# Optimization experiments

Hardware: AMD Instinct MI355X
Metric: run time of the kernel (lower is better)

The kernel has to match this reference:

```python
import jax, jax.numpy as jnp
import numpy as np

B, T, C = 4, 2048, 1024
NQ, D = 8, C // 8  # n_query heads, head dim = n_embd // 8


def setup_inputs() -> dict:
    key = jax.random.key(0)
    ks = jax.random.split(key, 6)
    s = 0.02
    return {
        "x": jax.random.normal(ks[0], (B, T, C), dtype=jnp.float32),
        "Wk": jax.random.normal(ks[1], (C, D), dtype=jnp.float32) * s,
        "Wv": jax.random.normal(ks[2], (C, D), dtype=jnp.float32) * s,
        "Wq": jax.random.normal(ks[3], (NQ, C, D), dtype=jnp.float32) * s,
        "Wp": jax.random.normal(ks[4], (NQ * D, C), dtype=jnp.float32) * s,
        "bp": jnp.zeros((C,), dtype=jnp.float32),
    }


def reference(x, Wk, Wv, Wq, Wp, bp):
    b, t, c = x.shape
    scale = c ** -0.5  # original scales by n_embd**-0.5, not head-dim
    k = x @ Wk                                   # [B,T,D] shared across heads (MQA)
    v = x @ Wv                                   # [B,T,D]
    q = jnp.einsum("btc,qcd->bqtd", x, Wq)       # [B,NQ,T,D]
    wei = jnp.einsum("bqtd,bsd->bqts", q, k) * scale
    causal = jnp.tril(jnp.ones((t, t), dtype=bool))
    wei = jnp.where(causal, wei, -jnp.inf)
    wei = jax.nn.softmax(wei, axis=-1)
    out = jnp.einsum("bqts,bsd->btqd", wei, v)   # [B,T,NQ,D]
    out = out.reshape(b, t, -1)                  # concat heads -> [B,T,NQ*D]
    return out @ Wp + bp
```

## Files before the change

kernel.cpp:

```cpp
#include <hip/hip_runtime.h>
#include <hip/hip_bf16.h>
#include <cstddef>
#include <cstdint>

#define B 4
#define T 2048
#define C 1024
#define NQ 8
#define D 128
#define M_ROWS (B * T)
#define NTOT (2 * D + NQ * D)

typedef __bf16 bf16x8 __attribute__((ext_vector_type(8)));
typedef float  f32x4  __attribute__((ext_vector_type(4)));
typedef uint32_t u32x4 __attribute__((ext_vector_type(4)));

__device__ __forceinline__ ushort f2bf(float f) {
    union { float f; uint32_t u; } v; v.f = f;
    const uint32_t r = (v.u + 0x7fffu + ((v.u >> 16) & 1u)) >> 16;
    return (ushort)r;
}

__device__ __forceinline__ uint32_t cvt_pk_bf16(float lo, float hi) {
    uint32_t r;
    asm("v_cvt_pk_bf16_f32 %0, %1, %2" : "=v"(r) : "v"(lo), "v"(hi));
    return r;
}

__device__ __forceinline__ void gld_lds16(const ushort* g, ushort* lds_uniform) {
    __builtin_amdgcn_global_load_lds(
        (const __attribute__((address_space(1))) void*)g,
        (__attribute__((address_space(3))) void*)lds_uniform, 16, 0, 0);
}

__global__ __launch_bounds__(256) void xcvt(const float* __restrict__ x,
                                            ushort* __restrict__ xb) {
    const size_t i = ((size_t)blockIdx.x * 256 + threadIdx.x) * 8;
    const float4 a = *(const float4*)(x + i);
    const float4 b = *(const float4*)(x + i + 4);
    uint4 o;
    o.x = f2bf(a.x) | ((uint32_t)f2bf(a.y) << 16);
    o.y = f2bf(a.z) | ((uint32_t)f2bf(a.w) << 16);
    o.z = f2bf(b.x) | ((uint32_t)f2bf(b.y) << 16);
    o.w = f2bf(b.z) | ((uint32_t)f2bf(b.w) << 16);
    *(uint4*)(xb + i) = o;
}

__device__ __forceinline__ void wtrans_body(const float* __restrict__ src,
                                            ushort* __restrict__ dst, int NC,
                                            int bx, int by) {
    __shared__ ushort Ts[64][72];
    const int tid = threadIdx.x;
    const int k0 = by * 64, c0 = bx * 64;
    {
        const int r = tid >> 2, cq = tid & 3;
#pragma unroll
        for (int i = 0; i < 4; ++i) {
            const int cc = cq * 16 + i * 4;
            const float4 v = *(const float4*)(src + (size_t)(k0 + r) * NC + c0 + cc);
            uint2 o;
            o.x = f2bf(v.x) | ((uint32_t)f2bf(v.y) << 16);
            o.y = f2bf(v.z) | ((uint32_t)f2bf(v.w) << 16);
            *(uint2*)(&Ts[r][cc]) = o;
        }
    }
    __syncthreads();
    {
        const int n = tid >> 2, kq = tid & 3;
        ushort vv[16];
#pragma unroll
        for (int j = 0; j < 16; ++j) vv[j] = Ts[kq * 16 + j][n];
        uint4 o0, o1;
        o0.x = vv[0] | ((uint32_t)vv[1] << 16);  o0.y = vv[2] | ((uint32_t)vv[3] << 16);
        o0.z = vv[4] | ((uint32_t)vv[5] << 16);  o0.w = vv[6] | ((uint32_t)vv[7] << 16);
        o1.x = vv[8] | ((uint32_t)vv[9] << 16);  o1.y = vv[10] | ((uint32_t)vv[11] << 16);
        o1.z = vv[12] | ((uint32_t)vv[13] << 16); o1.w = vv[14] | ((uint32_t)vv[15] << 16);
        ushort* d = dst + (size_t)(c0 + n) * C + k0 + kq * 16;
        *(uint4*)d = o0;
        *(uint4*)(d + 8) = o1;
    }
}

__global__ __launch_bounds__(256) void wtrans_qkv(const float* __restrict__ Wk,
                                                  const float* __restrict__ Wv,
                                                  const float* __restrict__ Wq,
                                                  ushort* __restrict__ WcatT) {
    const int z = blockIdx.z;
    const float* src;
    int rbase;
    if (z == 0)      { src = Wk; rbase = 0; }
    else if (z == 1) { src = Wv; rbase = D; }
    else             { src = Wq + (size_t)(z - 2) * C * D; rbase = 2 * D + (z - 2) * D; }
    wtrans_body(src, WcatT + (size_t)rbase * C, D, blockIdx.x, blockIdx.y);
}

__global__ __launch_bounds__(256) void wtrans_p(const float* __restrict__ Wp,
                                                ushort* __restrict__ WpT) {
    wtrans_body(Wp, WpT, C, blockIdx.x, blockIdx.y);
}

__global__ __launch_bounds__(256) void vtrans(const ushort* __restrict__ qkv,
                                              ushort* __restrict__ vbT) {
    __shared__ ushort Ts[64][136];
    const int tid = threadIdx.x;
    const int kb0 = blockIdx.x * 64;
    {
        const int r = tid >> 2, cq = tid & 3;
        const ushort* src = qkv + (size_t)(kb0 + r) * NTOT + D;
#pragma unroll
        for (int i = 0; i < 4; ++i) {
            const int cc = (cq * 4 + i) * 8;
            *(uint4*)(&Ts[r][cc]) = *(const uint4*)(src + cc);
        }
    }
    __syncthreads();
    {
        const int d = tid >> 1, half = tid & 1;
        ushort vv[32];
#pragma unroll
        for (int k = 0; k < 32; ++k) vv[k] = Ts[half * 32 + k][d];
        uint32_t dw[16];
#pragma unroll
        for (int i = 0; i < 16; ++i) {
            const int p0 = 2 * i, p1 = 2 * i + 1;
            const int k0 = (p0 & 3) | (((p0 >> 3) & 3) << 2) | (((p0 >> 2) & 1) << 4);
            const int k1 = (p1 & 3) | (((p1 >> 3) & 3) << 2) | (((p1 >> 2) & 1) << 4);
            dw[i] = vv[k0] | ((uint32_t)vv[k1] << 16);
        }
        uint32_t* dst = (uint32_t*)(vbT + (size_t)d * M_ROWS + kb0 + half * 32);
#pragma unroll
        for (int i = 0; i < 4; ++i)
            *(uint4*)(dst + i * 4) = *(uint4*)(&dw[i * 4]);
    }
}

template <bool BF16_OUT>
__global__ __launch_bounds__(256) void gemm_mfma(const ushort* __restrict__ A,
                                                 const ushort* __restrict__ Bt,
                                                 void* __restrict__ Cout,
                                                 const float* __restrict__ bias,
                                                 const int Nout) {
    __shared__ ushort As[128 * 32];
    __shared__ ushort Bs[128 * 32];
    const int tid  = threadIdx.x;
    const int lane = tid & 63;
    const int w    = tid >> 6;
    const int col  = lane & 15;
    const int quad = lane >> 4;
    const int row0 = blockIdx.y * 128;
    const int col0 = blockIdx.x * 128;
    const int wm = w & 1, wn = w >> 1;

    const int srow = lane >> 2;
    const int skk  = (lane & 3) * 8;

    f32x4 acc[4][4];
#pragma unroll
    for (int i = 0; i < 4; ++i)
#pragma unroll
        for (int j = 0; j < 4; ++j) acc[i][j] = (f32x4){0.f, 0.f, 0.f, 0.f};

    for (int k0 = 0; k0 < C; k0 += 32) {
        __syncthreads();
#pragma unroll
        for (int j = 0; j < 2; ++j) {
            const int ci = w * 2 + j;
            const int r  = ci * 16 + srow;
            gld_lds16(A  + (size_t)(row0 + r) * C + k0 + skk, &As[ci * 512]);
            gld_lds16(Bt + (size_t)(col0 + r) * C + k0 + skk, &Bs[ci * 512]);
        }
        __syncthreads();

        bf16x8 af[4], bfr[4];
#pragma unroll
        for (int i = 0; i < 4; ++i)
            af[i] = *(const bf16x8*)&As[(wm * 64 + i * 16 + col) * 32 + quad * 8];
#pragma unroll
        for (int j = 0; j < 4; ++j)
            bfr[j] = *(const bf16x8*)&Bs[(wn * 64 + j * 16 + col) * 32 + quad * 8];
#pragma unroll
        for (int i = 0; i < 4; ++i)
#pragma unroll
            for (int j = 0; j < 4; ++j)
                acc[i][j] = __builtin_amdgcn_mfma_f32_16x16x32_bf16(af[i], bfr[j], acc[i][j], 0, 0, 0);
    }

#pragma unroll
    for (int i = 0; i < 4; ++i) {
#pragma unroll
        for (int r = 0; r < 4; ++r) {
            const int grow = row0 + wm * 64 + i * 16 + quad * 4 + r;
#pragma unroll
            for (int j = 0; j < 4; ++j) {
                const int gcol = col0 + wn * 64 + j * 16 + col;
                const float v = acc[i][j][r];
                if (BF16_OUT) {
                    ((ushort*)Cout)[(size_t)grow * Nout + gcol] = f2bf(v);
                } else {
                    ((float*)Cout)[(size_t)grow * Nout + gcol] = v + bias[gcol];
                }
            }
        }
    }
}

__global__ __launch_bounds__(256, 2) void attn_mfma(const ushort* __restrict__ qkv,
                                                    const ushort* __restrict__ vbT,
                                                    ushort* __restrict__ attb) {
    __shared__ ushort Ks[2][4][64][32];
    __shared__ ushort Vt[2][4][128][16];

    const int tid  = threadIdx.x;
    const int lane = tid & 63;
    const int w    = tid >> 6;
    const int col  = lane & 15;
    const int quad = lane >> 4;
    const int h    = blockIdx.y;
    const int b    = blockIdx.z;
    const int qb_i = ((b >> 1) & 1) ? (gridDim.x - 1 - blockIdx.x) : blockIdx.x;
    const int q0   = qb_i * 128;

    bf16x8 qf[2][4];
#pragma unroll
    for (int qs = 0; qs < 2; ++qs) {
        const ushort* qrow = qkv + (size_t)(b * T + q0 + w * 32 + qs * 16 + col) * NTOT + 2 * D + h * D;
#pragma unroll
        for (int kb2 = 0; kb2 < 4; ++kb2)
            qf[qs][kb2] = *(const bf16x8*)(qrow + kb2 * 32 + quad * 8);
    }

    const ushort* kbase = qkv + (size_t)b * T * NTOT;
    const ushort* vbase = vbT + (size_t)b * T;

    f32x4 O[2][8];
#pragma unroll
    for (int qs = 0; qs < 2; ++qs)
#pragma unroll
        for (int i = 0; i < 8; ++i) O[qs][i] = (f32x4){0.f, 0.f, 0.f, 0.f};
    float l_acc[2] = {0.f, 0.f};

    const int ntiles  = 2 * qb_i + 2;
    const int sk_key  = lane >> 2;
    const int sk_d    = (lane & 3) * 8;
    const int sv_d    = lane >> 1;
    const int sv_half = (lane & 1) * 8;
    const int kg0     = quad >> 1;
    const int ko      = (quad & 1) * 8;
    const float SC = 0.045084220f;

    auto stage = [&](int it, int bufi) {
        const int s0 = it * 64;
#pragma unroll
        for (int kg = 0; kg < 4; ++kg)
            gld_lds16(kbase + (size_t)(s0 + kg * 16 + sk_key) * NTOT + w * 32 + sk_d,
                      &Ks[bufi][w][kg * 16][0]);
#pragma unroll
        for (int i2 = 0; i2 < 4; ++i2)
            gld_lds16(vbase + (size_t)(i2 * 32 + sv_d) * M_ROWS + s0 + w * 16 + sv_half,
                      &Vt[bufi][w][i2 * 32][0]);
    };

    int cur = 0;
    stage(0, 0);
    __syncthreads();

    for (int it = 0; it < ntiles; ++it) {
        if (it + 1 < ntiles) stage(it + 1, cur ^ 1);

        const bool active = (w >= 2) || (it < ntiles - 1);
        if (active) {
            const int s0 = it * 64;

            f32x4 S[2][4];
#pragma unroll
            for (int qs = 0; qs < 2; ++qs)
#pragma unroll
                for (int sub = 0; sub < 4; ++sub) S[qs][sub] = (f32x4){0.f, 0.f, 0.f, 0.f};
#pragma unroll
            for (int sub = 0; sub < 4; ++sub) {
#pragma unroll
                for (int kb2 = 0; kb2 < 4; ++kb2) {
                    bf16x8 kf = *(const bf16x8*)(&Ks[cur][kb2][sub * 16 + col][quad * 8]);
                    S[0][sub] = __builtin_amdgcn_mfma_f32_16x16x32_bf16(kf, qf[0][kb2], S[0][sub], 0, 0, 0);
                    S[1][sub] = __builtin_amdgcn_mfma_f32_16x16x32_bf16(kf, qf[1][kb2], S[1][sub], 0, 0, 0);
                }
            }

            const bool diag = (it >= ntiles - 2);
            bf16x8 paf[2][2];
#pragma unroll
            for (int qs = 0; qs < 2; ++qs) {
                float p[4][4];
                if (diag) {
                    const int q = q0 + w * 32 + qs * 16 + col;
#pragma unroll
                    for (int sub = 0; sub < 4; ++sub)
#pragma unroll
                        for (int r = 0; r < 4; ++r) {
                            const int key = s0 + sub * 16 + quad * 4 + r;
                            const float sc = (key > q) ? -1e30f : S[qs][sub][r] * SC;
                            p[sub][r] = __builtin_amdgcn_exp2f(sc);
                        }
                } else {
#pragma unroll
                    for (int sub = 0; sub < 4; ++sub)
#pragma unroll
                        for (int r = 0; r < 4; ++r)
                            p[sub][r] = __builtin_amdgcn_exp2f(S[qs][sub][r] * SC);
                }
                float ls = 0.f;
#pragma unroll
                for (int sub = 0; sub < 4; ++sub)
                    ls += (p[sub][0] + p[sub][1]) + (p[sub][2] + p[sub][3]);
                l_acc[qs] += ls;

                u32x4 w0, w1;
                w0.x = cvt_pk_bf16(p[0][0], p[0][1]);
                w0.y = cvt_pk_bf16(p[0][2], p[0][3]);
                w0.z = cvt_pk_bf16(p[1][0], p[1][1]);
                w0.w = cvt_pk_bf16(p[1][2], p[1][3]);
                w1.x = cvt_pk_bf16(p[2][0], p[2][1]);
                w1.y = cvt_pk_bf16(p[2][2], p[2][3]);
                w1.z = cvt_pk_bf16(p[3][0], p[3][1]);
                w1.w = cvt_pk_bf16(p[3][2], p[3][3]);
                paf[qs][0] = __builtin_bit_cast(bf16x8, w0);
                paf[qs][1] = __builtin_bit_cast(bf16x8, w1);
            }

#pragma unroll
            for (int nt = 0; nt < 8; ++nt) {
                bf16x8 vf0 = *(const bf16x8*)(&Vt[cur][kg0][nt * 16 + col][ko]);
                bf16x8 vf1 = *(const bf16x8*)(&Vt[cur][2 + kg0][nt * 16 + col][ko]);
#pragma unroll
                for (int qs = 0; qs < 2; ++qs) {
                    O[qs][nt] = __builtin_amdgcn_mfma_f32_16x16x32_bf16(paf[qs][0], vf0, O[qs][nt], 0, 0, 0);
                    O[qs][nt] = __builtin_amdgcn_mfma_f32_16x16x32_bf16(paf[qs][1], vf1, O[qs][nt], 0, 0, 0);
                }
            }
        }

        __syncthreads();
        cur ^= 1;
    }

#pragma unroll
    for (int qs = 0; qs < 2; ++qs) {
        float s = l_acc[qs];
        s += __shfl_xor(s, 16);
        s += __shfl_xor(s, 32);
#pragma unroll
        for (int r = 0; r < 4; ++r) {
            const float inv = 1.0f / __shfl(s, quad * 4 + r);
            const int t = q0 + w * 32 + qs * 16 + quad * 4 + r;
            ushort* orow = attb + (size_t)(b * T + t) * C + h * D;
#pragma unroll
            for (int nt = 0; nt < 8; ++nt)
                orow[nt * 16 + col] = f2bf(O[qs][nt][r] * inv);
        }
    }
}

extern "C" void kernel_launch(void* const* d_in, const int* in_sizes, int n_in,
                              void* d_out, int out_size, void* d_ws, size_t ws_size,
                              hipStream_t stream) {
    const float* x  = (const float*)d_in[0];
    const float* Wk = (const float*)d_in[1];
    const float* Wv = (const float*)d_in[2];
    const float* Wq = (const float*)d_in[3];
    const float* Wp = (const float*)d_in[4];
    const float* bp = (const float*)d_in[5];
    float* out = (float*)d_out;

    char* ws = (char*)d_ws;
    ushort* xb    = (ushort*)ws;
    ushort* attb  = xb;
    ushort* qkv   = (ushort*)(ws + (size_t)16  * 1024 * 1024);
    ushort* WcatT = (ushort*)(ws + (size_t)36  * 1024 * 1024);
    ushort* WpT   = (ushort*)(ws + (size_t)39  * 1024 * 1024);
    ushort* vbT   = (ushort*)(ws + (size_t)41  * 1024 * 1024);

    xcvt<<<(size_t)M_ROWS * C / (256 * 8), 256, 0, stream>>>(x, xb);
    wtrans_qkv<<<dim3(D / 64, C / 64, 2 + NQ), 256, 0, stream>>>(Wk, Wv, Wq, WcatT);
    wtrans_p<<<dim3(C / 64, C / 64), 256, 0, stream>>>(Wp, WpT);

    gemm_mfma<true><<<dim3(NTOT / 128, M_ROWS / 128), 256, 0, stream>>>(
        xb, WcatT, qkv, nullptr, NTOT);

    vtrans<<<M_ROWS / 64, 256, 0, stream>>>(qkv, vbT);

    attn_mfma<<<dim3(T / 128, NQ, B), 256, 0, stream>>>(qkv, vbT, attb);

    gemm_mfma<false><<<dim3(C / 128, M_ROWS / 128), 256, 0, stream>>>(
        attb, WpT, out, bp, C);
}
```

Before: 211.6 us.

## Use two waves per attention block with 64 query rows each

```diff
diff --git a/kernel.cpp b/kernel.cpp
--- a/kernel.cpp
+++ b/kernel.cpp
@@ -204,7 +204,7 @@
     }
 }
 
-__global__ __launch_bounds__(256, 2) void attn_mfma(const ushort* __restrict__ qkv,
+__global__ __launch_bounds__(128, 2) void attn_mfma(const ushort* __restrict__ qkv,
                                                     const ushort* __restrict__ vbT,
                                                     ushort* __restrict__ attb) {
     __shared__ ushort Ks[2][4][64][32];
@@ -217,13 +217,13 @@
     const int quad = lane >> 4;
     const int h    = blockIdx.y;
     const int b    = blockIdx.z;
-    const int qb_i = ((b >> 1) & 1) ? (gridDim.x - 1 - blockIdx.x) : blockIdx.x;
+    const int qb_i = ((b >> 1) & 1) ? (15 - (int)blockIdx.x) : (int)blockIdx.x;
     const int q0   = qb_i * 128;
 
-    bf16x8 qf[2][4];
-#pragma unroll
-    for (int qs = 0; qs < 2; ++qs) {
-        const ushort* qrow = qkv + (size_t)(b * T + q0 + w * 32 + qs * 16 + col) * NTOT + 2 * D + h * D;
+    bf16x8 qf[4][4];
+#pragma unroll
+    for (int qs = 0; qs < 4; ++qs) {
+        const ushort* qrow = qkv + (size_t)(b * T + q0 + w * 64 + qs * 16 + col) * NTOT + 2 * D + h * D;
 #pragma unroll
         for (int kb2 = 0; kb2 < 4; ++kb2)
             qf[qs][kb2] = *(const bf16x8*)(qrow + kb2 * 32 + quad * 8);
@@ -232,12 +232,12 @@
     const ushort* kbase = qkv + (size_t)b * T * NTOT;
     const ushort* vbase = vbT + (size_t)b * T;
 
-    f32x4 O[2][8];
-#pragma unroll
-    for (int qs = 0; qs < 2; ++qs)
+    f32x4 O[4][8];
+#pragma unroll
+    for (int qs = 0; qs < 4; ++qs)
 #pragma unroll
         for (int i = 0; i < 8; ++i) O[qs][i] = (f32x4){0.f, 0.f, 0.f, 0.f};
-    float l_acc[2] = {0.f, 0.f};
+    float l_acc[4] = {0.f, 0.f, 0.f, 0.f};
 
     const int ntiles  = 2 * qb_i + 2;
     const int sk_key  = lane >> 2;
@@ -251,13 +251,17 @@
     auto stage = [&](int it, int bufi) {
         const int s0 = it * 64;
 #pragma unroll
-        for (int kg = 0; kg < 4; ++kg)
-            gld_lds16(kbase + (size_t)(s0 + kg * 16 + sk_key) * NTOT + w * 32 + sk_d,
-                      &Ks[bufi][w][kg * 16][0]);
-#pragma unroll
-        for (int i2 = 0; i2 < 4; ++i2)
-            gld_lds16(vbase + (size_t)(i2 * 32 + sv_d) * M_ROWS + s0 + w * 16 + sv_half,
-                      &Vt[bufi][w][i2 * 32][0]);
+        for (int cc = 0; cc < 2; ++cc) {
+            const int c = w * 2 + cc;
+#pragma unroll
+            for (int kg = 0; kg < 4; ++kg)
+                gld_lds16(kbase + (size_t)(s0 + kg * 16 + sk_key) * NTOT + c * 32 + sk_d,
+                          &Ks[bufi][c][kg * 16][0]);
+#pragma unroll
+            for (int i2 = 0; i2 < 4; ++i2)
+                gld_lds16(vbase + (size_t)(i2 * 32 + sv_d) * M_ROWS + s0 + c * 16 + sv_half,
+                          &Vt[bufi][c][i2 * 32][0]);
+        }
     };
 
     int cur = 0;
@@ -267,76 +271,70 @@
     for (int it = 0; it < ntiles; ++it) {
         if (it + 1 < ntiles) stage(it + 1, cur ^ 1);
 
-        const bool active = (w >= 2) || (it < ntiles - 1);
-        if (active) {
+        const bool skip = (w == 0) && (it == ntiles - 1);
+        if (!skip) {
             const int s0 = it * 64;
-
-            f32x4 S[2][4];
-#pragma unroll
-            for (int qs = 0; qs < 2; ++qs)
-#pragma unroll
-                for (int sub = 0; sub < 4; ++sub) S[qs][sub] = (f32x4){0.f, 0.f, 0.f, 0.f};
-#pragma unroll
-            for (int sub = 0; sub < 4; ++sub) {
-#pragma unroll
-                for (int kb2 = 0; kb2 < 4; ++kb2) {
-                    bf16x8 kf = *(const bf16x8*)(&Ks[cur][kb2][sub * 16 + col][quad * 8]);
-                    S[0][sub] = __builtin_amdgcn_mfma_f32_16x16x32_bf16(kf, qf[0][kb2], S[0][sub], 0, 0, 0);
-                    S[1][sub] = __builtin_amdgcn_mfma_f32_16x16x32_bf16(kf, qf[1][kb2], S[1][sub], 0, 0, 0);
+            const bool diag = (it == ntiles - 2 + w);
+
+#pragma unroll
+            for (int hf = 0; hf < 2; ++hf) {
+                f32x4 S[4][2];
+#pragma unroll
+                for (int qs = 0; qs < 4; ++qs)
+#pragma unroll
+                    for (int sub = 0; sub < 2; ++sub) S[qs][sub] = (f32x4){0.f, 0.f, 0.f, 0.f};
+#pragma unroll
+                for (int sub = 0; sub < 2; ++sub) {
+#pragma unroll
+                    for (int kb2 = 0; kb2 < 4; ++kb2) {
+                        bf16x8 kf = *(const bf16x8*)(&Ks[cur][kb2][hf * 32 + sub * 16 + col][quad * 8]);
+                        S[0][sub] = __builtin_amdgcn_mfma_f32_16x16x32_bf16(kf, qf[0][kb2], S[0][sub], 0, 0, 0);
+                        S[1][sub] = __builtin_amdgcn_mfma_f32_16x16x32_bf16(kf, qf[1][kb2], S[1][sub], 0, 0, 0);
+                        S[2][sub] = __builtin_amdgcn_mfma_f32_16x16x32_bf16(kf, qf[2][kb2], S[2][sub], 0, 0, 0);
+                        S[3][sub] = __builtin_amdgcn_mfma_f32_16x16x32_bf16(kf, qf[3][kb2], S[3][sub], 0, 0, 0);
+                    }
+                }
+
+                bf16x8 paf[4];
+#pragma unroll
+                for (int qs = 0; qs < 4; ++qs) {
+                    float p[2][4];
+                    if (diag) {
+                        const int q = q0 + w * 64 + qs * 16 + col;
+#pragma unroll
+                        for (int sub = 0; sub < 2; ++sub)
+#pragma unroll
+                            for (int r = 0; r < 4; ++r) {
+                                const int key = s0 + hf * 32 + sub * 16 + quad * 4 + r;
+                                const float sc = (key > q) ? -1e30f : S[qs][sub][r] * SC;
+                                p[sub][r] = __builtin_amdgcn_exp2f(sc);
+                            }
+                    } else {
+#pragma unroll
+                        for (int sub = 0; sub < 2; ++sub)
+#pragma unroll
+                            for (int r = 0; r < 4; ++r)
+                                p[sub][r] = __builtin_amdgcn_exp2f(S[qs][sub][r] * SC);
+                    }
+                    l_acc[qs] += (p[0][0] + p[0][1]) + (p[0][2] + p[0][3])
+                               + (p[1][0] + p[1][1]) + (p[1][2] + p[1][3]);
+                    u32x4 wpk;
+                    wpk.x = cvt_pk_bf16(p[0][0], p[0][1]);
+                    wpk.y = cvt_pk_bf16(p[0][2], p[0][3]);
+                    wpk.z = cvt_pk_bf16(p[1][0], p[1][1]);
+                    wpk.w = cvt_pk_bf16(p[1][2], p[1][3]);
+                    paf[qs] = __builtin_bit_cast(bf16x8, wpk);
+                }
+
+#pragma unroll
+                for (int nt = 0; nt < 8; ++nt) {
+                    bf16x8 vf = *(const bf16x8*)(&Vt[cur][hf * 2 + kg0][nt * 16 + col][ko]);
+                    O[0][nt] = __builtin_amdgcn_mfma_f32_16x16x32_bf16(paf[0], vf, O[0][nt], 0, 0, 0);
+                    O[1][nt] = __builtin_amdgcn_mfma_f32_16x16x32_bf16(paf[1], vf, O[1][nt], 0, 0, 0);
+                    O[2][nt] = __builtin_amdgcn_mfma_f32_16x16x32_bf16(paf[2], vf, O[2][nt], 0, 0, 0);
+                    O[3][nt] = __builtin_amdgcn_mfma_f32_16x16x32_bf16(paf[3], vf, O[3][nt], 0, 0, 0);
                 }
             }
-
-            const bool diag = (it >= ntiles - 2);
-            bf16x8 paf[2][2];
-#pragma unroll
-            for (int qs = 0; qs < 2; ++qs) {
-                float p[4][4];
-                if (diag) {
-                    const int q = q0 + w * 32 + qs * 16 + col;
-#pragma unroll
-                    for (int sub = 0; sub < 4; ++sub)
-#pragma unroll
-                        for (int r = 0; r < 4; ++r) {
-                            const int key = s0 + sub * 16 + quad * 4 + r;
-                            const float sc = (key > q) ? -1e30f : S[qs][sub][r] * SC;
-                            p[sub][r] = __builtin_amdgcn_exp2f(sc);
-                        }
-                } else {
-#pragma unroll
-                    for (int sub = 0; sub < 4; ++sub)
-#pragma unroll
-                        for (int r = 0; r < 4; ++r)
-                            p[sub][r] = __builtin_amdgcn_exp2f(S[qs][sub][r] * SC);
-                }
-                float ls = 0.f;
-#pragma unroll
-                for (int sub = 0; sub < 4; ++sub)
-                    ls += (p[sub][0] + p[sub][1]) + (p[sub][2] + p[sub][3]);
-                l_acc[qs] += ls;
-
-                u32x4 w0, w1;
-                w0.x = cvt_pk_bf16(p[0][0], p[0][1]);
-                w0.y = cvt_pk_bf16(p[0][2], p[0][3]);
-                w0.z = cvt_pk_bf16(p[1][0], p[1][1]);
-                w0.w = cvt_pk_bf16(p[1][2], p[1][3]);
-                w1.x = cvt_pk_bf16(p[2][0], p[2][1]);
-                w1.y = cvt_pk_bf16(p[2][2], p[2][3]);
-                w1.z = cvt_pk_bf16(p[3][0], p[3][1]);
-                w1.w = cvt_pk_bf16(p[3][2], p[3][3]);
-                paf[qs][0] = __builtin_bit_cast(bf16x8, w0);
-                paf[qs][1] = __builtin_bit_cast(bf16x8, w1);
-            }
-
-#pragma unroll
-            for (int nt = 0; nt < 8; ++nt) {
-                bf16x8 vf0 = *(const bf16x8*)(&Vt[cur][kg0][nt * 16 + col][ko]);
-                bf16x8 vf1 = *(const bf16x8*)(&Vt[cur][2 + kg0][nt * 16 + col][ko]);
-#pragma unroll
-                for (int qs = 0; qs < 2; ++qs) {
-                    O[qs][nt] = __builtin_amdgcn_mfma_f32_16x16x32_bf16(paf[qs][0], vf0, O[qs][nt], 0, 0, 0);
-                    O[qs][nt] = __builtin_amdgcn_mfma_f32_16x16x32_bf16(paf[qs][1], vf1, O[qs][nt], 0, 0, 0);
-                }
-            }
         }
 
         __syncthreads();
@@ -344,14 +342,14 @@
     }
 
 #pragma unroll
-    for (int qs = 0; qs < 2; ++qs) {
+    for (int qs = 0; qs < 4; ++qs) {
         float s = l_acc[qs];
         s += __shfl_xor(s, 16);
         s += __shfl_xor(s, 32);
 #pragma unroll
         for (int r = 0; r < 4; ++r) {
             const float inv = 1.0f / __shfl(s, quad * 4 + r);
-            const int t = q0 + w * 32 + qs * 16 + quad * 4 + r;
+            const int t = q0 + w * 64 + qs * 16 + quad * 4 + r;
             ushort* orow = attb + (size_t)(b * T + t) * C + h * D;
 #pragma unroll
             for (int nt = 0; nt < 8; ++nt)
@@ -388,7 +386,7 @@
 
     vtrans<<<M_ROWS / 64, 256, 0, stream>>>(qkv, vbT);
 
-    attn_mfma<<<dim3(T / 128, NQ, B), 256, 0, stream>>>(qkv, vbT, attb);
+    attn_mfma<<<dim3(T / 128, NQ, B), 128, 0, stream>>>(qkv, vbT, attb);
 
     gemm_mfma<false><<<dim3(C / 128, M_ROWS / 128), 256, 0, stream>>>(
         attb, WpT, out, bp, C);
```

After: 274.5 us. +29.8%, slower.
